# Performance work log

Measured on AMD Instinct MI355X. Metric: run time of the kernel, lower is better.

## Reference

```python
import jax, jax.numpy as jnp
import numpy as np


def setup_inputs() -> dict:
    key = jax.random.key(0)
    k1, k2 = jax.random.split(key)
    B, C, M, N = 8, 3, 4096, 4096
    pc_src = jax.random.normal(k1, (B, C, M), dtype=jnp.float32)
    pc_dst = jax.random.normal(k2, (B, C, N), dtype=jnp.float32)
    return {"pc_src": pc_src, "pc_dst": pc_dst}


def reference(pc_src, pc_dst):
    # pc_src: [B,3,M], pc_dst: [B,3,N]
    # Pairwise Euclidean distance via ||s||^2 + ||d||^2 - 2 s.d (avoids Bx3xMxN tensor)
    s2 = jnp.sum(pc_src * pc_src, axis=1)              # [B,M]
    d2 = jnp.sum(pc_dst * pc_dst, axis=1)              # [B,N]
    cross = jnp.einsum('bcm,bcn->bmn', pc_src, pc_dst)  # [B,M,N]
    sq = s2[:, :, None] + d2[:, None, :] - 2.0 * cross
    diff = jnp.sqrt(jnp.maximum(sq, 0.0))              # [B,M,N] L2 distances
    forward_loss = jnp.mean(jnp.min(diff, axis=2))     # src -> dst nearest
    backward_loss = jnp.mean(jnp.min(diff, axis=1))    # dst -> src nearest
    chamfer_pure = forward_loss + backward_loss
    chamfer_weighted = chamfer_pure
    return (forward_loss + backward_loss, chamfer_pure, chamfer_weighted)
```

## Files before the change

### kernel.cpp

```cpp
#include <hip/hip_runtime.h>
#include <math.h>


constexpr int B = 8;
constexpr int M = 4096;

typedef __attribute__((ext_vector_type(8)))  short bf16x8;
typedef __attribute__((ext_vector_type(16))) float f32x16;

__device__ inline unsigned short bf16_of(float x) {
    unsigned int u = __float_as_uint(x);
    u += 0x7FFFu + ((u >> 16) & 1u);
    return (unsigned short)(u >> 16);
}
__device__ inline float bf16_to_f(unsigned short h) {
    return __uint_as_float(((unsigned int)h) << 16);
}

__device__ inline float tree_min16(const f32x16 a) {
    const float t0 = fminf(a[0],  a[1]);
    const float t1 = fminf(a[2],  a[3]);
    const float t2 = fminf(a[4],  a[5]);
    const float t3 = fminf(a[6],  a[7]);
    const float t4 = fminf(a[8],  a[9]);
    const float t5 = fminf(a[10], a[11]);
    const float t6 = fminf(a[12], a[13]);
    const float t7 = fminf(a[14], a[15]);
    const float u0 = fminf(t0, t1);
    const float u1 = fminf(t2, t3);
    const float u2 = fminf(t4, t5);
    const float u3 = fminf(t6, t7);
    return fminf(fminf(u0, u1), fminf(u2, u3));
}


__global__ __launch_bounds__(256, 4) void chamfer_main(
    const float* __restrict__ src,
    const float* __restrict__ dst,
    float* __restrict__ part)
{
    int bid = blockIdx.x;
    const int cs  = bid & 1;  bid >>= 1;
    const int rg  = bid & 31; bid >>= 5;
    const int b   = bid & 7;  bid >>= 3;
    const int dir = bid;

    const float* __restrict__ qry = dir ? dst : src;
    const float* __restrict__ ref = dir ? src : dst;

    const int tid  = threadIdx.x;
    const int wave = tid >> 6;
    const int l31  = tid & 31;
    const int hf   = (tid >> 5) & 1;

    __shared__ __align__(16) unsigned short bstage[2][1024][8];

    const int sA = l31 ^ (l31 >> 3);
    const int sB = 32 + (l31 ^ (4 | (l31 >> 3)));

    bf16x8 afrag;
    {
        const int mrow = rg * 128 + wave * 32 + l31;
        const float* qb = qry + (size_t)b * 3 * M;
        const float x = qb[0 * M + mrow];
        const float y = qb[1 * M + mrow];
        const float z = qb[2 * M + mrow];
        const float s2 = x * x + y * y + z * z;
        const float xhf = bf16_to_f(bf16_of(x));
        const float yhf = bf16_to_f(bf16_of(y));
        const float zhf = bf16_to_f(bf16_of(z));
        const unsigned short nxh = bf16_of(-2.0f * xhf), nxl = bf16_of(-2.0f * (x - xhf));
        const unsigned short nyh = bf16_of(-2.0f * yhf), nyl = bf16_of(-2.0f * (y - yhf));
        const unsigned short nzh = bf16_of(-2.0f * zhf), nzl = bf16_of(-2.0f * (z - zhf));
        const unsigned short s2h = bf16_of(s2);
        const unsigned short s2l = bf16_of(s2 - bf16_to_f(s2h));
        const unsigned short one = 0x3F80;
        bf16x8 alo, ahi;
        alo[0]=(short)nxh; alo[1]=(short)nxh; alo[2]=(short)nxl; alo[3]=(short)nxl;
        alo[4]=(short)nyh; alo[5]=(short)nyh; alo[6]=(short)nyl; alo[7]=(short)nyl;
        ahi[0]=(short)nzh; ahi[1]=(short)nzh; ahi[2]=(short)nzl; ahi[3]=(short)nzl;
        ahi[4]=(short)s2h; ahi[5]=(short)s2l; ahi[6]=(short)one; ahi[7]=(short)one;
        afrag = hf ? ahi : alo;
    }

    float fwdE = 3.0e38f, fwdO = 3.0e38f;

    const f32x16 zero = {};
    const float* rb = ref + (size_t)b * 3 * M + cs * 2048;

    for (int ch = 0; ch < 2; ++ch) {
        __syncthreads();
        {
            const int c0 = tid * 4;
            const float4 vx = *reinterpret_cast<const float4*>(&rb[0 * M + ch * 1024 + c0]);
            const float4 vy = *reinterpret_cast<const float4*>(&rb[1 * M + ch * 1024 + c0]);
            const float4 vz = *reinterpret_cast<const float4*>(&rb[2 * M + ch * 1024 + c0]);
            const float xs[4] = {vx.x, vx.y, vx.z, vx.w};
            const float ys[4] = {vy.x, vy.y, vy.z, vy.w};
            const float zs[4] = {vz.x, vz.y, vz.z, vz.w};
#pragma unroll
            for (int k = 0; k < 4; ++k) {
                const float x = xs[k], y = ys[k], z = zs[k];
                const float d2 = x * x + y * y + z * z;
                const unsigned short xh = bf16_of(x), xl = bf16_of(x - bf16_to_f(xh));
                const unsigned short yh = bf16_of(y), yl = bf16_of(y - bf16_to_f(yh));
                const unsigned short zh = bf16_of(z), zl = bf16_of(z - bf16_to_f(zh));
                const unsigned short d2h = bf16_of(d2);
                const unsigned short d2l = bf16_of(d2 - bf16_to_f(d2h));
                const unsigned short one = 0x3F80;
                bf16x8 v0, v1;
                v0[0]=(short)xh; v0[1]=(short)xl; v0[2]=(short)xh; v0[3]=(short)xl;
                v0[4]=(short)yh; v0[5]=(short)yl; v0[6]=(short)yh; v0[7]=(short)yl;
                v1[0]=(short)zh; v1[1]=(short)zl; v1[2]=(short)zh; v1[3]=(short)zl;
                v1[4]=(short)one; v1[5]=(short)one; v1[6]=(short)d2h; v1[7]=(short)d2l;
                const int c = c0 + k;
                const int swz = c ^ ((c >> 3) & 7);
                *reinterpret_cast<bf16x8*>(&bstage[0][swz][0]) = v0;
                *reinterpret_cast<bf16x8*>(&bstage[1][swz][0]) = v1;
            }
        }
        __syncthreads();

#pragma unroll 4
        for (int i = 0; i < 16; ++i) {
            const bf16x8 bf0 = *reinterpret_cast<const bf16x8*>(&bstage[hf][i * 64 + sA][0]);
            const bf16x8 bf1 = *reinterpret_cast<const bf16x8*>(&bstage[hf][i * 64 + sB][0]);
            const f32x16 acc0 = __builtin_amdgcn_mfma_f32_32x32x16_bf16(bf0, afrag, zero, 0, 0, 0);
            const f32x16 acc1 = __builtin_amdgcn_mfma_f32_32x32x16_bf16(bf1, afrag, zero, 0, 0, 0);
            fwdE = fminf(fwdE, tree_min16(acc0));
            fwdO = fminf(fwdO, tree_min16(acc1));
        }
    }

    float v = fminf(fwdE, fwdO);
    v = fminf(v, __shfl_xor(v, 32));
    if (hf == 0) {
        part[((size_t)cs * 16 + dir * 8 + b) * M + rg * 128 + wave * 32 + l31] = v;
    }
}

__global__ __launch_bounds__(256) void chamfer_reduce(
    const float* __restrict__ part, float* __restrict__ bsums)
{
    const int idx = blockIdx.x * 256 + threadIdx.x;
    const int row = idx & (M - 1);
    const int db  = idx >> 12;

    const float* p = part + (size_t)db * M + row;
    const float v = fminf(p[0], p[(size_t)16 * M]);

    float s = sqrtf(fmaxf(v, 0.0f));
#pragma unroll
    for (int off = 32; off > 0; off >>= 1) s += __shfl_down(s, off);
    __shared__ float partial[4];
    if ((threadIdx.x & 63) == 0) partial[threadIdx.x >> 6] = s;
    __syncthreads();
    if (threadIdx.x == 0)
        bsums[blockIdx.x] = partial[0] + partial[1] + partial[2] + partial[3];
}

__global__ __launch_bounds__(256) void chamfer_final(
    const float* __restrict__ bsums, float* __restrict__ out)
{
    float s = bsums[threadIdx.x];
#pragma unroll
    for (int off = 32; off > 0; off >>= 1) s += __shfl_down(s, off);
    __shared__ float partial[4];
    if ((threadIdx.x & 63) == 0) partial[threadIdx.x >> 6] = s;
    __syncthreads();
    if (threadIdx.x == 0) {
        const float tot = (partial[0] + partial[1] + partial[2] + partial[3])
                        * (1.0f / (float)(B * M));
        out[0] = tot;
        out[1] = tot;
        out[2] = tot;
    }
}

extern "C" void kernel_launch(void* const* d_in, const int* in_sizes, int n_in,
                              void* d_out, int out_size, void* d_ws, size_t ws_size,
                              hipStream_t stream)
{
    const float* src = (const float*)d_in[0];
    const float* dst = (const float*)d_in[1];
    float* out = (float*)d_out;

    float* part  = (float*)d_ws;
    float* bsums = (float*)((char*)d_ws + (1u << 19));

    chamfer_main  <<<1024, 256, 0, stream>>>(src, dst, part);
    chamfer_reduce<<<256, 256, 0, stream>>>(part, bsums);
    chamfer_final <<<1, 256, 0, stream>>>(bsums, out);
}
```

Measured before the change: 23.96 us.

## Give each wave two query fragments and split reference into four chunks

Each wave now holds two 32-row query fragments and reuses every staged reference fragment across both, doing four MFMAs per LDS read pair instead of two. The reference set is split into four 1024-point chunks per block rather than two, so each block stages one chunk and drops the inner chunk loop and its extra barriers. The partial-min buffer grows to four slices, the reduce kernel takes the min over four values, and the workspace offset for the block sums moves to make room. This halves LDS traffic per MFMA and the block-level sync overhead, at the cost of more registers and more partial writes.

```diff
diff --git a/kernel.cpp b/kernel.cpp
--- a/kernel.cpp
+++ b/kernel.cpp
@@ -33,6 +33,28 @@
     return fminf(fminf(u0, u1), fminf(u2, u3));
 }
 
+__device__ inline bf16x8 make_qfrag(const float* qb, int row, int hf) {
+    const float x = qb[0 * M + row];
+    const float y = qb[1 * M + row];
+    const float z = qb[2 * M + row];
+    const float s2 = x * x + y * y + z * z;
+    const float xhf = bf16_to_f(bf16_of(x));
+    const float yhf = bf16_to_f(bf16_of(y));
+    const float zhf = bf16_to_f(bf16_of(z));
+    const unsigned short nxh = bf16_of(-2.0f * xhf), nxl = bf16_of(-2.0f * (x - xhf));
+    const unsigned short nyh = bf16_of(-2.0f * yhf), nyl = bf16_of(-2.0f * (y - yhf));
+    const unsigned short nzh = bf16_of(-2.0f * zhf), nzl = bf16_of(-2.0f * (z - zhf));
+    const unsigned short s2h = bf16_of(s2);
+    const unsigned short s2l = bf16_of(s2 - bf16_to_f(s2h));
+    const unsigned short one = 0x3F80;
+    bf16x8 alo, ahi;
+    alo[0]=(short)nxh; alo[1]=(short)nxh; alo[2]=(short)nxl; alo[3]=(short)nxl;
+    alo[4]=(short)nyh; alo[5]=(short)nyh; alo[6]=(short)nyl; alo[7]=(short)nyl;
+    ahi[0]=(short)nzh; ahi[1]=(short)nzh; ahi[2]=(short)nzl; ahi[3]=(short)nzl;
+    ahi[4]=(short)s2h; ahi[5]=(short)s2l; ahi[6]=(short)one; ahi[7]=(short)one;
+    return hf ? ahi : alo;
+}
+
 
 __global__ __launch_bounds__(256, 4) void chamfer_main(
     const float* __restrict__ src,
@@ -40,8 +62,8 @@
     float* __restrict__ part)
 {
     int bid = blockIdx.x;
-    const int cs  = bid & 1;  bid >>= 1;
-    const int rg  = bid & 31; bid >>= 5;
+    const int cs  = bid & 3;  bid >>= 2;
+    const int rg  = bid & 15; bid >>= 4;
     const int b   = bid & 7;  bid >>= 3;
     const int dir = bid;
 
@@ -58,84 +80,70 @@
     const int sA = l31 ^ (l31 >> 3);
     const int sB = 32 + (l31 ^ (4 | (l31 >> 3)));
 
-    bf16x8 afrag;
+    const int rbase = rg * 256 + wave * 64;
+    const float* qb = qry + (size_t)b * 3 * M;
+    const bf16x8 qf0 = make_qfrag(qb, rbase + l31,      hf);
+    const bf16x8 qf1 = make_qfrag(qb, rbase + 32 + l31, hf);
+
+    float fwdE0 = 3.0e38f, fwdO0 = 3.0e38f;
+    float fwdE1 = 3.0e38f, fwdO1 = 3.0e38f;
+
+    const f32x16 zero = {};
+    const float* rb = ref + (size_t)b * 3 * M + cs * 1024;
+
     {
-        const int mrow = rg * 128 + wave * 32 + l31;
-        const float* qb = qry + (size_t)b * 3 * M;
-        const float x = qb[0 * M + mrow];
-        const float y = qb[1 * M + mrow];
-        const float z = qb[2 * M + mrow];
-        const float s2 = x * x + y * y + z * z;
-        const float xhf = bf16_to_f(bf16_of(x));
-        const float yhf = bf16_to_f(bf16_of(y));
-        const float zhf = bf16_to_f(bf16_of(z));
-        const unsigned short nxh = bf16_of(-2.0f * xhf), nxl = bf16_of(-2.0f * (x - xhf));
-        const unsigned short nyh = bf16_of(-2.0f * yhf), nyl = bf16_of(-2.0f * (y - yhf));
-        const unsigned short nzh = bf16_of(-2.0f * zhf), nzl = bf16_of(-2.0f * (z - zhf));
-        const unsigned short s2h = bf16_of(s2);
-        const unsigned short s2l = bf16_of(s2 - bf16_to_f(s2h));
-        const unsigned short one = 0x3F80;
-        bf16x8 alo, ahi;
-        alo[0]=(short)nxh; alo[1]=(short)nxh; alo[2]=(short)nxl; alo[3]=(short)nxl;
-        alo[4]=(short)nyh; alo[5]=(short)nyh; alo[6]=(short)nyl; alo[7]=(short)nyl;
-        ahi[0]=(short)nzh; ahi[1]=(short)nzh; ahi[2]=(short)nzl; ahi[3]=(short)nzl;
-        ahi[4]=(short)s2h; ahi[5]=(short)s2l; ahi[6]=(short)one; ahi[7]=(short)one;
-        afrag = hf ? ahi : alo;
-    }
-
-    float fwdE = 3.0e38f, fwdO = 3.0e38f;
-
-    const f32x16 zero = {};
-    const float* rb = ref + (size_t)b * 3 * M + cs * 2048;
-
-    for (int ch = 0; ch < 2; ++ch) {
-        __syncthreads();
-        {
-            const int c0 = tid * 4;
-            const float4 vx = *reinterpret_cast<const float4*>(&rb[0 * M + ch * 1024 + c0]);
-            const float4 vy = *reinterpret_cast<const float4*>(&rb[1 * M + ch * 1024 + c0]);
-            const float4 vz = *reinterpret_cast<const float4*>(&rb[2 * M + ch * 1024 + c0]);
-            const float xs[4] = {vx.x, vx.y, vx.z, vx.w};
-            const float ys[4] = {vy.x, vy.y, vy.z, vy.w};
-            const float zs[4] = {vz.x, vz.y, vz.z, vz.w};
+        const int c0 = tid * 4;
+        const float4 vx = *reinterpret_cast<const float4*>(&rb[0 * M + c0]);
+        const float4 vy = *reinterpret_cast<const float4*>(&rb[1 * M + c0]);
+        const float4 vz = *reinterpret_cast<const float4*>(&rb[2 * M + c0]);
+        const float xs[4] = {vx.x, vx.y, vx.z, vx.w};
+        const float ys[4] = {vy.x, vy.y, vy.z, vy.w};
+        const float zs[4] = {vz.x, vz.y, vz.z, vz.w};
 #pragma unroll
-            for (int k = 0; k < 4; ++k) {
-                const float x = xs[k], y = ys[k], z = zs[k];
-                const float d2 = x * x + y * y + z * z;
-                const unsigned short xh = bf16_of(x), xl = bf16_of(x - bf16_to_f(xh));
-                const unsigned short yh = bf16_of(y), yl = bf16_of(y - bf16_to_f(yh));
-                const unsigned short zh = bf16_of(z), zl = bf16_of(z - bf16_to_f(zh));
-                const unsigned short d2h = bf16_of(d2);
-                const unsigned short d2l = bf16_of(d2 - bf16_to_f(d2h));
-                const unsigned short one = 0x3F80;
-                bf16x8 v0, v1;
-                v0[0]=(short)xh; v0[1]=(short)xl; v0[2]=(short)xh; v0[3]=(short)xl;
-                v0[4]=(short)yh; v0[5]=(short)yl; v0[6]=(short)yh; v0[7]=(short)yl;
-                v1[0]=(short)zh; v1[1]=(short)zl; v1[2]=(short)zh; v1[3]=(short)zl;
-                v1[4]=(short)one; v1[5]=(short)one; v1[6]=(short)d2h; v1[7]=(short)d2l;
-                const int c = c0 + k;
-                const int swz = c ^ ((c >> 3) & 7);
-                *reinterpret_cast<bf16x8*>(&bstage[0][swz][0]) = v0;
-                *reinterpret_cast<bf16x8*>(&bstage[1][swz][0]) = v1;
-            }
+        for (int k = 0; k < 4; ++k) {
+            const float x = xs[k], y = ys[k], z = zs[k];
+            const float d2 = x * x + y * y + z * z;
+            const unsigned short xh = bf16_of(x), xl = bf16_of(x - bf16_to_f(xh));
+            const unsigned short yh = bf16_of(y), yl = bf16_of(y - bf16_to_f(yh));
+            const unsigned short zh = bf16_of(z), zl = bf16_of(z - bf16_to_f(zh));
+            const unsigned short d2h = bf16_of(d2);
+            const unsigned short d2l = bf16_of(d2 - bf16_to_f(d2h));
+            const unsigned short one = 0x3F80;
+            bf16x8 v0, v1;
+            v0[0]=(short)xh; v0[1]=(short)xl; v0[2]=(short)xh; v0[3]=(short)xl;
+            v0[4]=(short)yh; v0[5]=(short)yl; v0[6]=(short)yh; v0[7]=(short)yl;
+            v1[0]=(short)zh; v1[1]=(short)zl; v1[2]=(short)zh; v1[3]=(short)zl;
+            v1[4]=(short)one; v1[5]=(short)one; v1[6]=(short)d2h; v1[7]=(short)d2l;
+            const int c = c0 + k;
+            const int swz = c ^ ((c >> 3) & 7);
+            *reinterpret_cast<bf16x8*>(&bstage[0][swz][0]) = v0;
+            *reinterpret_cast<bf16x8*>(&bstage[1][swz][0]) = v1;
         }
-        __syncthreads();
+    }
+    __syncthreads();
 
 #pragma unroll 4
-        for (int i = 0; i < 16; ++i) {
-            const bf16x8 bf0 = *reinterpret_cast<const bf16x8*>(&bstage[hf][i * 64 + sA][0]);
-            const bf16x8 bf1 = *reinterpret_cast<const bf16x8*>(&bstage[hf][i * 64 + sB][0]);
-            const f32x16 acc0 = __builtin_amdgcn_mfma_f32_32x32x16_bf16(bf0, afrag, zero, 0, 0, 0);
-            const f32x16 acc1 = __builtin_amdgcn_mfma_f32_32x32x16_bf16(bf1, afrag, zero, 0, 0, 0);
-            fwdE = fminf(fwdE, tree_min16(acc0));
-            fwdO = fminf(fwdO, tree_min16(acc1));
-        }
-    }
-
-    float v = fminf(fwdE, fwdO);
-    v = fminf(v, __shfl_xor(v, 32));
+    for (int i = 0; i < 16; ++i) {
+        const bf16x8 bf0 = *reinterpret_cast<const bf16x8*>(&bstage[hf][i * 64 + sA][0]);
+        const bf16x8 bf1 = *reinterpret_cast<const bf16x8*>(&bstage[hf][i * 64 + sB][0]);
+        const f32x16 a00 = __builtin_amdgcn_mfma_f32_32x32x16_bf16(bf0, qf0, zero, 0, 0, 0);
+        fwdE0 = fminf(fwdE0, tree_min16(a00));
+        const f32x16 a01 = __builtin_amdgcn_mfma_f32_32x32x16_bf16(bf0, qf1, zero, 0, 0, 0);
+        fwdE1 = fminf(fwdE1, tree_min16(a01));
+        const f32x16 a10 = __builtin_amdgcn_mfma_f32_32x32x16_bf16(bf1, qf0, zero, 0, 0, 0);
+        fwdO0 = fminf(fwdO0, tree_min16(a10));
+        const f32x16 a11 = __builtin_amdgcn_mfma_f32_32x32x16_bf16(bf1, qf1, zero, 0, 0, 0);
+        fwdO1 = fminf(fwdO1, tree_min16(a11));
+    }
+
+    float v0 = fminf(fwdE0, fwdO0);
+    float v1 = fminf(fwdE1, fwdO1);
+    v0 = fminf(v0, __shfl_xor(v0, 32));
+    v1 = fminf(v1, __shfl_xor(v1, 32));
     if (hf == 0) {
-        part[((size_t)cs * 16 + dir * 8 + b) * M + rg * 128 + wave * 32 + l31] = v;
+        float* pf = part + ((size_t)cs * 16 + dir * 8 + b) * M + rbase;
+        pf[l31]      = v0;
+        pf[32 + l31] = v1;
     }
 }
 
@@ -147,7 +155,8 @@
     const int db  = idx >> 12;
 
     const float* p = part + (size_t)db * M + row;
-    const float v = fminf(p[0], p[(size_t)16 * M]);
+    const float v = fminf(fminf(p[0],              p[(size_t)16 * M]),
+                          fminf(p[(size_t)32 * M], p[(size_t)48 * M]));
 
     float s = sqrtf(fmaxf(v, 0.0f));
 #pragma unroll
@@ -186,7 +195,7 @@
     float* out = (float*)d_out;
 
     float* part  = (float*)d_ws;
-    float* bsums = (float*)((char*)d_ws + (1u << 19));
+    float* bsums = (float*)((char*)d_ws + (1u << 20));
 
     chamfer_main  <<<1024, 256, 0, stream>>>(src, dst, part);
     chamfer_reduce<<<256, 256, 0, stream>>>(part, bsums);
```

Result: no change. 23.99 us (+0.2%).
